# Kernel optimization log

Hardware: AMD Instinct MI355X
Metric: run time of the kernel (lower is better)

Reference implementation:

```python
import jax, jax.numpy as jnp
import numpy as np

B, L, HID = 2, 2048, 4096
NH, NKV, HD = 16, 4, 64
BLOCK = 16
THETA = 8000000.0
EPS = 1e-6
NEG = jnp.finfo(jnp.float32).min


def _rope_tables(theta, L, hd):
    inv_freq = 1.0 / (theta ** (np.arange(0, hd, 2, dtype=np.float32) / hd))  # [hd/2]
    t = np.arange(L, dtype=np.float32)
    freqs = np.outer(t, inv_freq)                      # [L, hd/2]
    emb = np.concatenate([freqs, freqs], axis=-1)      # [L, hd]
    return jnp.asarray(np.cos(emb)), jnp.asarray(np.sin(emb))


def setup_inputs() -> dict:
    key = jax.random.key(0)
    k1, k2, k3 = jax.random.split(key, 3)
    hidden_states = jax.random.normal(k1, (B, L, HID), dtype=jnp.float32)
    Wqkv = jax.random.normal(k2, (HID, (NH + 2 * NKV) * HD), dtype=jnp.float32) * 0.006
    Wo = jax.random.normal(k3, (NH * HD, HID), dtype=jnp.float32) * 0.006
    q_norm_w = jnp.ones((HD,), dtype=jnp.float32)
    k_norm_w = jnp.ones((HD,), dtype=jnp.float32)
    # block-diagonal causal additive mask [1,1,L,L]
    idx = jnp.arange(L)
    same_block = (idx[:, None] // BLOCK) == (idx[None, :] // BLOCK)
    causal = idx[:, None] >= idx[None, :]
    attention_mask = jnp.where(same_block & causal, 0.0, NEG)[None, None].astype(jnp.float32)
    cos1, sin1 = _rope_tables(THETA, L, HD)
    cos = jnp.broadcast_to(cos1[None], (B, L, HD))
    sin = jnp.broadcast_to(sin1[None], (B, L, HD))
    return {"hidden_states": hidden_states, "attention_mask": attention_mask,
            "cos": cos, "sin": sin, "Wqkv": Wqkv, "Wo": Wo,
            "q_norm_w": q_norm_w, "k_norm_w": k_norm_w}


def _rms_norm(x, w):
    xf = x.astype(jnp.float32)
    var = jnp.mean(xf * xf, axis=-1, keepdims=True)
    return (xf * jax.lax.rsqrt(var + EPS)).astype(x.dtype) * w


def _rotate_half(x):
    x1, x2 = jnp.split(x, 2, axis=-1)
    return jnp.concatenate([-x2, x1], axis=-1)


def reference(hidden_states, attention_mask, cos, sin, Wqkv, Wo, q_norm_w, k_norm_w):
    Bc, Lc, _ = hidden_states.shape
    qkv = hidden_states @ Wqkv                                # [B,L,(NH+2NKV)*HD]
    qkv = qkv.reshape(Bc, Lc, NH + 2 * NKV, HD)
    q, k, v = jnp.split(qkv, [NH, NH + NKV], axis=2)
    q = q.transpose(0, 2, 1, 3)                               # [B,NH,L,HD]
    k = k.transpose(0, 2, 1, 3)                               # [B,NKV,L,HD]
    v = v.transpose(0, 2, 1, 3)
    q = _rms_norm(q, q_norm_w)
    k = _rms_norm(k, k_norm_w)
    c = cos[:, None]                                          # [B,1,L,HD]
    s = sin[:, None]
    q = q * c + _rotate_half(q) * s
    k = k * c + _rotate_half(k) * s
    groups = NH // NKV
    k = jnp.repeat(k, groups, axis=1)                         # [B,NH,L,HD]
    v = jnp.repeat(v, groups, axis=1)
    scale = 1.0 / jnp.sqrt(jnp.float32(HD))
    scores = jnp.einsum('bhqd,bhkd->bhqk', q, k) * scale + attention_mask
    probs = jax.nn.softmax(scores, axis=-1)
    out = jnp.einsum('bhqk,bhkd->bhqd', probs, v)             # [B,NH,L,HD]
    out = out.transpose(0, 2, 1, 3).reshape(Bc, Lc, NH * HD)
    return out @ Wo
```

## Files before the change

kernel.cpp:

```cpp
#include <hip/hip_runtime.h>
#include <hip/hip_bf16.h>
#include <cstdint>

#define B_SZ   2
#define L_SEQ  2048
#define HID    4096
#define NH     16
#define NKV    4
#define HD     64
#define NQKV   (NH + 2*NKV)
#define QKV_N  (NQKV*HD)
#define O_N    (NH*HD)
#define M_ROWS (B_SZ*L_SEQ)
#define EPSV   1e-6f

typedef __bf16  bf16x8_t  __attribute__((ext_vector_type(8)));
typedef float   f32x4_t   __attribute__((ext_vector_type(4)));
typedef unsigned short ushort8_t __attribute__((ext_vector_type(8)));

__device__ __forceinline__ unsigned short f2b(float f) {
    union { float f; uint32_t u; } v; v.f = f;
    uint32_t r = v.u + 0x7FFFu + ((v.u >> 16) & 1u);
    return (unsigned short)(r >> 16);
}

__device__ __forceinline__ void gload_lds16(const void* g, void* l) {
    __builtin_amdgcn_global_load_lds(
        (__attribute__((address_space(1))) void*)(g),
        (__attribute__((address_space(3))) void*)(l),
        16, 0, 0);
}

#define BARF() do { asm volatile("" ::: "memory"); \
                    __builtin_amdgcn_s_barrier();  \
                    asm volatile("" ::: "memory"); } while (0)
#define LGKM0() do { asm volatile("s_waitcnt lgkmcnt(0)" ::: "memory"); \
                     __builtin_amdgcn_sched_barrier(0); } while (0)
#define VMC4()  asm volatile("s_waitcnt vmcnt(4)" ::: "memory")
#define VMC0()  asm volatile("s_waitcnt vmcnt(0)" ::: "memory")

__global__ __launch_bounds__(256) void cvt_f32_bf16(const float* __restrict__ in,
                                                    unsigned short* __restrict__ out,
                                                    int n8) {
    int i = blockIdx.x * 256 + threadIdx.x;
    if (i >= n8) return;
    const float4* p = (const float4*)(in + (size_t)i * 8);
    float4 a = p[0], b = p[1];
    ushort8_t o;
    o[0]=f2b(a.x); o[1]=f2b(a.y); o[2]=f2b(a.z); o[3]=f2b(a.w);
    o[4]=f2b(b.x); o[5]=f2b(b.y); o[6]=f2b(b.z); o[7]=f2b(b.w);
    *(ushort8_t*)(out + (size_t)i * 8) = o;
}

__global__ __launch_bounds__(256) void transpose_f32_bf16(const float* __restrict__ in,
                                                          unsigned short* __restrict__ out,
                                                          int R, int C) {
    __shared__ float t[32][33];
    const int c0 = blockIdx.x * 32;
    const int r0 = blockIdx.y * 32;
    const int tx = threadIdx.x & 31;
    const int ty = threadIdx.x >> 5;
    #pragma unroll
    for (int i = 0; i < 32; i += 8)
        t[ty + i][tx] = in[(size_t)(r0 + ty + i) * C + c0 + tx];
    __syncthreads();
    #pragma unroll
    for (int i = 0; i < 32; i += 8)
        out[(size_t)(c0 + ty + i) * R + r0 + tx] = f2b(t[tx][ty + i]);
}

__global__ __launch_bounds__(512, 2) void gemm256_bf16(const unsigned short* __restrict__ A,
                                                       const unsigned short* __restrict__ Bt,
                                                       float* __restrict__ C,
                                                       int M, int N, int K) {
    __shared__ unsigned short smem[65536];

    const int tid  = threadIdx.x;
    const int lane = tid & 63;
    const int wave = tid >> 6;
    const int wr   = wave >> 2;
    const int wc   = wave & 3;
    const int fr   = lane & 15;
    const int fq   = lane >> 4;

    const int nbx = N >> 8;
    int bid = blockIdx.x;
    const int cpx = gridDim.x >> 3;
    bid = (bid & 7) * cpx + (bid >> 3);
    const int bx = bid % nbx, by = bid / nbx;
    const int m0 = by << 8, n0 = bx << 8;

    const int srow = tid >> 3;
    const int scs  = ((tid & 7) ^ (srow & 7)) << 3;
    const unsigned short* gA = A  + (size_t)(m0 + srow) * K + scs;
    const unsigned short* gB = Bt + (size_t)(n0 + srow) * K + scs;

    const int cx0 = ((fq)     ^ (fr & 7)) << 3;
    const int cx1 = ((4 | fq) ^ (fr & 7)) << 3;

    f32x4_t acc[8][4];
    #pragma unroll
    for (int m = 0; m < 8; m++)
        #pragma unroll
        for (int n = 0; n < 4; n++)
            acc[m][n] = (f32x4_t){0.f, 0.f, 0.f, 0.f};

    bf16x8_t aF[2][2];
    bf16x8_t bF[4][2];

#define STG_A2(T, H) { _Pragma("unroll") for (int q = 0; q < 2; ++q) \
    gload_lds16(gA + (size_t)((H)*128 + q*64) * K + ((size_t)(T) << 6), \
                &smem[(((T)&1)<<15) + ((H)*128 + q*64)*64 + tid*8]); }
#define STG_B2(T, H) { _Pragma("unroll") for (int q = 0; q < 2; ++q) \
    gload_lds16(gB + (size_t)((H)*128 + q*64) * K + ((size_t)(T) << 6), \
                &smem[(((T)&1)<<15) + 16384 + ((H)*128 + q*64)*64 + tid*8]); }
#define RD_B2(SB) { _Pragma("unroll") for (int nn = 0; nn < 4; ++nn) { \
    const int ro = (SB) + 16384 + (wc*64 + nn*16 + fr)*64; \
    bF[nn][0] = *(const bf16x8_t*)&smem[ro + cx0]; \
    bF[nn][1] = *(const bf16x8_t*)&smem[ro + cx1]; } }
#define RD_A2(SB, P) { _Pragma("unroll") for (int m2 = 0; m2 < 2; ++m2) { \
    const int ro = (SB) + (wr*128 + ((P)*2 + m2)*16 + fr)*64; \
    aF[m2][0] = *(const bf16x8_t*)&smem[ro + cx0]; \
    aF[m2][1] = *(const bf16x8_t*)&smem[ro + cx1]; } }
#define MM2(P) { __builtin_amdgcn_s_setprio(1); \
    _Pragma("unroll") for (int m2 = 0; m2 < 2; ++m2) \
    _Pragma("unroll") for (int nn = 0; nn < 4; ++nn) \
    _Pragma("unroll") for (int kk = 0; kk < 2; ++kk) \
        acc[(P)*2 + m2][nn] = __builtin_amdgcn_mfma_f32_16x16x32_bf16( \
            aF[m2][kk], bF[nn][kk], acc[(P)*2 + m2][nn], 0, 0, 0); \
    __builtin_amdgcn_s_setprio(0); }

    const int NT = K >> 6;
    STG_A2(0, 0); STG_A2(0, 1); STG_B2(0, 0); STG_B2(0, 1);
    STG_B2(1, 0); STG_B2(1, 1);
    VMC4();
    BARF();

    for (int t = 0; t < NT; ++t) {
        const int sb = (t & 1) << 15;
        RD_B2(sb); RD_A2(sb, 0);
        if (t + 1 < NT) STG_A2(t + 1, 0);
        BARF(); LGKM0(); MM2(0); BARF();
        RD_A2(sb, 1);
        if (t + 1 < NT) STG_A2(t + 1, 1);
        BARF(); LGKM0(); MM2(1); BARF();
        RD_A2(sb, 2);
        if (t + 2 < NT) STG_B2(t + 2, 0);
        BARF(); LGKM0(); MM2(2); BARF();
        RD_A2(sb, 3);
        if (t + 2 < NT) STG_B2(t + 2, 1);
        BARF(); LGKM0(); MM2(3);
        if (t + 2 < NT) { VMC4(); } else { VMC0(); }
        BARF();
    }

    const int crow = m0 + wr * 128 + fq * 4;
    const int ccol = n0 + wc * 64 + fr;
    #pragma unroll
    for (int m = 0; m < 8; m++)
        #pragma unroll
        for (int n = 0; n < 4; n++)
            #pragma unroll
            for (int rr = 0; rr < 4; rr++)
                C[(size_t)(crow + m*16 + rr) * N + ccol + n*16] = acc[m][n][rr];
#undef STG_A2
#undef STG_B2
#undef RD_B2
#undef RD_A2
#undef MM2
}

__global__ __launch_bounds__(512, 2) void gemm256x128_bf16(const unsigned short* __restrict__ A,
                                                           const unsigned short* __restrict__ Bt,
                                                           float* __restrict__ C,
                                                           int M, int N, int K) {
    __shared__ unsigned short smem[49152];

    const int tid  = threadIdx.x;
    const int lane = tid & 63;
    const int wave = tid >> 6;
    const int wq   = wave >> 1;
    const int wn   = wave & 1;
    const int fr   = lane & 15;
    const int fq   = lane >> 4;

    const int nbx = N >> 7;
    int bid = blockIdx.x;
    const int cpx = gridDim.x >> 3;
    bid = (bid & 7) * cpx + (bid >> 3);
    const int bx = bid % nbx, by = bid / nbx;
    const int m0 = by << 8, n0 = bx << 7;

    const int srow = tid >> 3;
    const int scs  = ((tid & 7) ^ (srow & 7)) << 3;
    const unsigned short* gA = A  + (size_t)(m0 + srow) * K + scs;
    const unsigned short* gB = Bt + (size_t)(n0 + srow) * K + scs;

    const int cx0 = ((fq)     ^ (fr & 7)) << 3;
    const int cx1 = ((4 | fq) ^ (fr & 7)) << 3;

    f32x4_t acc[4][4];
    #pragma unroll
    for (int m = 0; m < 4; m++)
        #pragma unroll
        for (int n = 0; n < 4; n++)
            acc[m][n] = (f32x4_t){0.f, 0.f, 0.f, 0.f};

    bf16x8_t aF[4][2];
    bf16x8_t bF[4][2];

#define STG_A1(T, H) { _Pragma("unroll") for (int q = 0; q < 2; ++q) \
    gload_lds16(gA + (size_t)((H)*128 + q*64) * K + ((size_t)(T) << 6), \
                &smem[((T)&1)*24576 + ((H)*128 + q*64)*64 + tid*8]); }
#define STG_B1(T) { _Pragma("unroll") for (int q = 0; q < 2; ++q) \
    gload_lds16(gB + (size_t)(q*64) * K + ((size_t)(T) << 6), \
                &smem[((T)&1)*24576 + 16384 + q*4096 + tid*8]); }
#define RD_A1(SB, MM) { _Pragma("unroll") for (int m2 = 0; m2 < 2; ++m2) { \
    const int ro = (SB) + (wq*64 + ((MM) + m2)*16 + fr)*64; \
    aF[(MM)+m2][0] = *(const bf16x8_t*)&smem[ro + cx0]; \
    aF[(MM)+m2][1] = *(const bf16x8_t*)&smem[ro + cx1]; } }
#define RD_B1(SB, NN) { _Pragma("unroll") for (int n2 = 0; n2 < 2; ++n2) { \
    const int ro = (SB) + 16384 + (wn*64 + ((NN) + n2)*16 + fr)*64; \
    bF[(NN)+n2][0] = *(const bf16x8_t*)&smem[ro + cx0]; \
    bF[(NN)+n2][1] = *(const bf16x8_t*)&smem[ro + cx1]; } }
#define MM1(MH, NH) { __builtin_amdgcn_s_setprio(1); \
    _Pragma("unroll") for (int m2 = 0; m2 < 2; ++m2) \
    _Pragma("unroll") for (int n2 = 0; n2 < 2; ++n2) \
    _Pragma("unroll") for (int kk = 0; kk < 2; ++kk) \
        acc[(MH)*2 + m2][(NH)*2 + n2] = __builtin_amdgcn_mfma_f32_16x16x32_bf16( \
            aF[(MH)*2 + m2][kk], bF[(NH)*2 + n2][kk], acc[(MH)*2 + m2][(NH)*2 + n2], 0, 0, 0); \
    __builtin_amdgcn_s_setprio(0); }

    const int NT = K >> 6;
    STG_A1(0, 0); STG_A1(0, 1); STG_B1(0);
    STG_B1(1); STG_A1(1, 0);
    VMC4();
    BARF();

    for (int t = 0; t < NT; ++t) {
        const int sb = (t & 1) * 24576;
        RD_A1(sb, 0); RD_B1(sb, 0);
        if (t + 1 < NT) STG_A1(t + 1, 1);
        BARF(); LGKM0(); MM1(0, 0); BARF();
        RD_B1(sb, 2);
        BARF(); LGKM0(); MM1(0, 1); BARF();
        RD_A1(sb, 2);
        if (t + 2 < NT) STG_B1(t + 2);
        BARF(); LGKM0(); MM1(1, 1); BARF();
        if (t + 2 < NT) STG_A1(t + 2, 0);
        BARF(); LGKM0(); MM1(1, 0);
        if (t + 2 < NT) { VMC4(); } else { VMC0(); }
        BARF();
    }

    const int crow = m0 + wq * 64 + fq * 4;
    const int ccol = n0 + wn * 64 + fr;
    #pragma unroll
    for (int m = 0; m < 4; m++)
        #pragma unroll
        for (int n = 0; n < 4; n++)
            #pragma unroll
            for (int rr = 0; rr < 4; rr++)
                C[(size_t)(crow + m*16 + rr) * N + ccol + n*16] = acc[m][n][rr];
#undef STG_A1
#undef STG_B1
#undef RD_A1
#undef RD_B1
#undef MM1
}

__global__ __launch_bounds__(64) void attn_fused(const float* __restrict__ qkv,
                                                 const float* __restrict__ cosb,
                                                 const float* __restrict__ sinb,
                                                 const float* __restrict__ qw,
                                                 const float* __restrict__ kw,
                                                 unsigned short* __restrict__ out) {
    const int h    = blockIdx.x & (NH - 1);
    const int blk  = (blockIdx.x >> 4) & 127;
    const int b    = blockIdx.x >> 11;
    const int pos0 = blk * 16;
    const int kvh  = h >> 2;

    const int lane = threadIdx.x;
    const int r    = lane >> 2;
    const int qp   = lane & 3;
    const int d0   = qp * 16;

    __shared__ float qs[16][65];
    __shared__ float ks[16][65];
    __shared__ float vs[16][65];
    __shared__ float ps[16][17];

    const size_t rowb = ((size_t)(b * L_SEQ + pos0 + r)) * NQKV;
    const float* qptr = qkv + (rowb + h) * HD + d0;
    const float* kptr = qkv + (rowb + NH + kvh) * HD + d0;
    const float* vptr = qkv + (rowb + NH + NKV + kvh) * HD + d0;
    const size_t csrow = ((size_t)(b * L_SEQ + pos0 + r)) * HD + d0;

    float q[16], k[16], v[16], cs[16], sn[16];
    #pragma unroll
    for (int i = 0; i < 16; i += 4) {
        *(float4*)&q[i]  = *(const float4*)&qptr[i];
        *(float4*)&k[i]  = *(const float4*)&kptr[i];
        *(float4*)&v[i]  = *(const float4*)&vptr[i];
        *(float4*)&cs[i] = *(const float4*)&cosb[csrow + i];
        *(float4*)&sn[i] = *(const float4*)&sinb[csrow + i];
    }

    float sq = 0.f, sk = 0.f;
    #pragma unroll
    for (int i = 0; i < 16; i++) { sq += q[i]*q[i]; sk += k[i]*k[i]; }
    sq += __shfl_xor(sq, 1); sq += __shfl_xor(sq, 2);
    sk += __shfl_xor(sk, 1); sk += __shfl_xor(sk, 2);
    const float rq = rsqrtf(sq * (1.f / HD) + EPSV);
    const float rk = rsqrtf(sk * (1.f / HD) + EPSV);

    const float sgn = (qp < 2) ? -1.f : 1.f;
    #pragma unroll
    for (int i = 0; i < 16; i++) {
        float qn = q[i] * rq * qw[d0 + i];
        float kn = k[i] * rk * kw[d0 + i];
        float qo = __shfl_xor(qn, 2);
        float ko = __shfl_xor(kn, 2);
        qs[r][d0 + i] = qn * cs[i] + sgn * qo * sn[i];
        ks[r][d0 + i] = kn * cs[i] + sgn * ko * sn[i];
        vs[r][d0 + i] = v[i];
    }
    __syncthreads();

    float sc[4] = {0.f, 0.f, 0.f, 0.f};
    for (int d = 0; d < 64; d++) {
        const float qd = qs[r][d];
        sc[0] += qd * ks[qp     ][d];
        sc[1] += qd * ks[qp +  4][d];
        sc[2] += qd * ks[qp +  8][d];
        sc[3] += qd * ks[qp + 12][d];
    }
    #pragma unroll
    for (int cc = 0; cc < 4; cc++) {
        const int c = qp + cc * 4;
        sc[cc] = (c <= r) ? sc[cc] * 0.125f : -3.0e38f;
    }
    float mx = fmaxf(fmaxf(sc[0], sc[1]), fmaxf(sc[2], sc[3]));
    mx = fmaxf(mx, __shfl_xor(mx, 1));
    mx = fmaxf(mx, __shfl_xor(mx, 2));
    float e[4], sum = 0.f;
    #pragma unroll
    for (int cc = 0; cc < 4; cc++) { e[cc] = __expf(sc[cc] - mx); sum += e[cc]; }
    sum += __shfl_xor(sum, 1); sum += __shfl_xor(sum, 2);
    const float inv = 1.f / sum;
    #pragma unroll
    for (int cc = 0; cc < 4; cc++) ps[r][qp + cc * 4] = e[cc] * inv;
    __syncthreads();

    float o[16];
    #pragma unroll
    for (int i = 0; i < 16; i++) o[i] = 0.f;
    #pragma unroll
    for (int c = 0; c < 16; c++) {
        const float p = ps[r][c];
        #pragma unroll
        for (int i = 0; i < 16; i++) o[i] += p * vs[c][d0 + i];
    }

    __attribute__((aligned(16))) unsigned short ob[16];
    #pragma unroll
    for (int i = 0; i < 16; i++) ob[i] = f2b(o[i]);
    unsigned short* optr = out + (((size_t)(b * L_SEQ + pos0 + r) * NH + h) * HD) + d0;
    *(uint4*)optr       = *(uint4*)&ob[0];
    *((uint4*)optr + 1) = *(uint4*)&ob[8];
}

extern "C" void kernel_launch(void* const* d_in, const int* in_sizes, int n_in,
                              void* d_out, int out_size, void* d_ws, size_t ws_size,
                              hipStream_t stream) {
    const float* hid  = (const float*)d_in[0];
    const float* cosb = (const float*)d_in[2];
    const float* sinb = (const float*)d_in[3];
    const float* Wqkv = (const float*)d_in[4];
    const float* Wo   = (const float*)d_in[5];
    const float* qw   = (const float*)d_in[6];
    const float* kw   = (const float*)d_in[7];
    float* outp = (float*)d_out;

    char* ws = (char*)d_ws;
    unsigned short* Hb    = (unsigned short*)ws; ws += (size_t)M_ROWS * HID * 2;
    unsigned short* WqkvT = (unsigned short*)ws; ws += (size_t)QKV_N * HID * 2;
    unsigned short* WoT   = (unsigned short*)ws; ws += (size_t)HID * O_N * 2;
    float*          qkvf  = (float*)ws;          ws += (size_t)M_ROWS * QKV_N * 4;
    unsigned short* attnb = (unsigned short*)ws;

    {
        int n8 = (M_ROWS * HID) / 8;
        cvt_f32_bf16<<<(n8 + 255) / 256, 256, 0, stream>>>(hid, Hb, n8);
    }
    transpose_f32_bf16<<<dim3(QKV_N / 32, HID / 32), 256, 0, stream>>>(Wqkv, WqkvT, HID, QKV_N);
    transpose_f32_bf16<<<dim3(HID / 32, O_N / 32),  256, 0, stream>>>(Wo,   WoT,   O_N, HID);
    gemm256x128_bf16<<<dim3((M_ROWS / 256) * (QKV_N / 128)), 512, 0, stream>>>(Hb, WqkvT, qkvf, M_ROWS, QKV_N, HID);
    attn_fused<<<dim3(B_SZ * (L_SEQ / 16) * NH), 64, 0, stream>>>(qkvf, cosb, sinb, qw, kw, attnb);
    gemm256_bf16<<<dim3((M_ROWS / 256) * (HID / 256)), 512, 0, stream>>>(attnb, WoT, outp, M_ROWS, HID, O_N);
}
```

Before: 161.8 us.

## Triple-buffer QKV GEMM pipeline and store QKV intermediate in bf16

The QKV GEMM moves from a two-stage LDS buffer with staggered A/B staging to a three-stage ring. Each stage is loaded whole two iterations ahead, so each k-step needs only two MFMA phases with fewer barriers, and all A fragments are loaded at once. The QKV output is now written as bf16 instead of fp32, which halves the intermediate traffic, and the attention kernel reads and unpacks bf16. In exchange, LDS use grows to 144KB per block, which may limit occupancy with launch bounds of (512,2), and q/k/v lose precision before the norm.

```diff
diff --git a/kernel.cpp b/kernel.cpp
--- a/kernel.cpp
+++ b/kernel.cpp
@@ -23,6 +23,10 @@
     uint32_t r = v.u + 0x7FFFu + ((v.u >> 16) & 1u);
     return (unsigned short)(r >> 16);
 }
+__device__ __forceinline__ float b2f(unsigned short u) {
+    union { uint32_t u; float f; } v; v.u = ((uint32_t)u) << 16;
+    return v.f;
+}
 
 __device__ __forceinline__ void gload_lds16(const void* g, void* l) {
     __builtin_amdgcn_global_load_lds(
@@ -36,6 +40,7 @@
                     asm volatile("" ::: "memory"); } while (0)
 #define LGKM0() do { asm volatile("s_waitcnt lgkmcnt(0)" ::: "memory"); \
                      __builtin_amdgcn_sched_barrier(0); } while (0)
+#define VMC6()  asm volatile("s_waitcnt vmcnt(6)" ::: "memory")
 #define VMC4()  asm volatile("s_waitcnt vmcnt(4)" ::: "memory")
 #define VMC0()  asm volatile("s_waitcnt vmcnt(0)" ::: "memory")
 
@@ -172,9 +177,9 @@
 
 __global__ __launch_bounds__(512, 2) void gemm256x128_bf16(const unsigned short* __restrict__ A,
                                                            const unsigned short* __restrict__ Bt,
-                                                           float* __restrict__ C,
+                                                           unsigned short* __restrict__ C,
                                                            int M, int N, int K) {
-    __shared__ unsigned short smem[49152];
+    __shared__ unsigned short smem[73728];
 
     const int tid  = threadIdx.x;
     const int lane = tid & 63;
@@ -207,49 +212,45 @@
             acc[m][n] = (f32x4_t){0.f, 0.f, 0.f, 0.f};
 
     bf16x8_t aF[4][2];
-    bf16x8_t bF[4][2];
-
-#define STG_A1(T, H) { _Pragma("unroll") for (int q = 0; q < 2; ++q) \
-    gload_lds16(gA + (size_t)((H)*128 + q*64) * K + ((size_t)(T) << 6), \
-                &smem[((T)&1)*24576 + ((H)*128 + q*64)*64 + tid*8]); }
-#define STG_B1(T) { _Pragma("unroll") for (int q = 0; q < 2; ++q) \
-    gload_lds16(gB + (size_t)(q*64) * K + ((size_t)(T) << 6), \
-                &smem[((T)&1)*24576 + 16384 + q*4096 + tid*8]); }
-#define RD_A1(SB, MM) { _Pragma("unroll") for (int m2 = 0; m2 < 2; ++m2) { \
-    const int ro = (SB) + (wq*64 + ((MM) + m2)*16 + fr)*64; \
-    aF[(MM)+m2][0] = *(const bf16x8_t*)&smem[ro + cx0]; \
-    aF[(MM)+m2][1] = *(const bf16x8_t*)&smem[ro + cx1]; } }
+    bf16x8_t bF[2][2];
+
+#define STG_T1(T) { const int pb = ((T)%3)*24576; \
+    _Pragma("unroll") for (int q = 0; q < 4; ++q) \
+        gload_lds16(gA + (size_t)(q*64)*K + ((size_t)(T) << 6), \
+                    &smem[pb + q*4096 + tid*8]); \
+    _Pragma("unroll") for (int q = 0; q < 2; ++q) \
+        gload_lds16(gB + (size_t)(q*64)*K + ((size_t)(T) << 6), \
+                    &smem[pb + 16384 + q*4096 + tid*8]); }
+#define RD_A1(SB) { _Pragma("unroll") for (int mm = 0; mm < 4; ++mm) { \
+    const int ro = (SB) + (wq*64 + mm*16 + fr)*64; \
+    aF[mm][0] = *(const bf16x8_t*)&smem[ro + cx0]; \
+    aF[mm][1] = *(const bf16x8_t*)&smem[ro + cx1]; } }
 #define RD_B1(SB, NN) { _Pragma("unroll") for (int n2 = 0; n2 < 2; ++n2) { \
     const int ro = (SB) + 16384 + (wn*64 + ((NN) + n2)*16 + fr)*64; \
-    bF[(NN)+n2][0] = *(const bf16x8_t*)&smem[ro + cx0]; \
-    bF[(NN)+n2][1] = *(const bf16x8_t*)&smem[ro + cx1]; } }
-#define MM1(MH, NH) { __builtin_amdgcn_s_setprio(1); \
-    _Pragma("unroll") for (int m2 = 0; m2 < 2; ++m2) \
+    bF[n2][0] = *(const bf16x8_t*)&smem[ro + cx0]; \
+    bF[n2][1] = *(const bf16x8_t*)&smem[ro + cx1]; } }
+#define MM1(NH_) { __builtin_amdgcn_s_setprio(1); \
+    _Pragma("unroll") for (int mm = 0; mm < 4; ++mm) \
     _Pragma("unroll") for (int n2 = 0; n2 < 2; ++n2) \
     _Pragma("unroll") for (int kk = 0; kk < 2; ++kk) \
-        acc[(MH)*2 + m2][(NH)*2 + n2] = __builtin_amdgcn_mfma_f32_16x16x32_bf16( \
-            aF[(MH)*2 + m2][kk], bF[(NH)*2 + n2][kk], acc[(MH)*2 + m2][(NH)*2 + n2], 0, 0, 0); \
+        acc[mm][(NH_)*2 + n2] = __builtin_amdgcn_mfma_f32_16x16x32_bf16( \
+            aF[mm][kk], bF[n2][kk], acc[mm][(NH_)*2 + n2], 0, 0, 0); \
     __builtin_amdgcn_s_setprio(0); }
 
     const int NT = K >> 6;
-    STG_A1(0, 0); STG_A1(0, 1); STG_B1(0);
-    STG_B1(1); STG_A1(1, 0);
-    VMC4();
+    STG_T1(0);
+    STG_T1(1);
+    VMC6();
     BARF();
 
     for (int t = 0; t < NT; ++t) {
-        const int sb = (t & 1) * 24576;
-        RD_A1(sb, 0); RD_B1(sb, 0);
-        if (t + 1 < NT) STG_A1(t + 1, 1);
-        BARF(); LGKM0(); MM1(0, 0); BARF();
+        const int sb = (t % 3) * 24576;
+        RD_A1(sb); RD_B1(sb, 0);
+        if (t + 2 < NT) STG_T1(t + 2);
+        BARF(); LGKM0(); MM1(0); BARF();
         RD_B1(sb, 2);
-        BARF(); LGKM0(); MM1(0, 1); BARF();
-        RD_A1(sb, 2);
-        if (t + 2 < NT) STG_B1(t + 2);
-        BARF(); LGKM0(); MM1(1, 1); BARF();
-        if (t + 2 < NT) STG_A1(t + 2, 0);
-        BARF(); LGKM0(); MM1(1, 0);
-        if (t + 2 < NT) { VMC4(); } else { VMC0(); }
+        BARF(); LGKM0(); MM1(1);
+        if (t + 2 < NT) { VMC6(); } else if (t + 1 < NT) { VMC0(); }
         BARF();
     }
 
@@ -261,15 +262,14 @@
         for (int n = 0; n < 4; n++)
             #pragma unroll
             for (int rr = 0; rr < 4; rr++)
-                C[(size_t)(crow + m*16 + rr) * N + ccol + n*16] = acc[m][n][rr];
-#undef STG_A1
-#undef STG_B1
+                C[(size_t)(crow + m*16 + rr) * N + ccol + n*16] = f2b(acc[m][n][rr]);
+#undef STG_T1
 #undef RD_A1
 #undef RD_B1
 #undef MM1
 }
 
-__global__ __launch_bounds__(64) void attn_fused(const float* __restrict__ qkv,
+__global__ __launch_bounds__(64) void attn_fused(const unsigned short* __restrict__ qkv,
                                                  const float* __restrict__ cosb,
                                                  const float* __restrict__ sinb,
                                                  const float* __restrict__ qw,
@@ -292,19 +292,27 @@
     __shared__ float ps[16][17];
 
     const size_t rowb = ((size_t)(b * L_SEQ + pos0 + r)) * NQKV;
-    const float* qptr = qkv + (rowb + h) * HD + d0;
-    const float* kptr = qkv + (rowb + NH + kvh) * HD + d0;
-    const float* vptr = qkv + (rowb + NH + NKV + kvh) * HD + d0;
+    const unsigned short* qptr = qkv + (rowb + h) * HD + d0;
+    const unsigned short* kptr = qkv + (rowb + NH + kvh) * HD + d0;
+    const unsigned short* vptr = qkv + (rowb + NH + NKV + kvh) * HD + d0;
     const size_t csrow = ((size_t)(b * L_SEQ + pos0 + r)) * HD + d0;
 
     float q[16], k[16], v[16], cs[16], sn[16];
-    #pragma unroll
-    for (int i = 0; i < 16; i += 4) {
-        *(float4*)&q[i]  = *(const float4*)&qptr[i];
-        *(float4*)&k[i]  = *(const float4*)&kptr[i];
-        *(float4*)&v[i]  = *(const float4*)&vptr[i];
-        *(float4*)&cs[i] = *(const float4*)&cosb[csrow + i];
-        *(float4*)&sn[i] = *(const float4*)&sinb[csrow + i];
+    {
+        ushort8_t q0 = *(const ushort8_t*)&qptr[0], q1 = *(const ushort8_t*)&qptr[8];
+        ushort8_t k0 = *(const ushort8_t*)&kptr[0], k1 = *(const ushort8_t*)&kptr[8];
+        ushort8_t v0 = *(const ushort8_t*)&vptr[0], v1 = *(const ushort8_t*)&vptr[8];
+        #pragma unroll
+        for (int i = 0; i < 8; i++) {
+            q[i] = b2f(q0[i]); q[i+8] = b2f(q1[i]);
+            k[i] = b2f(k0[i]); k[i+8] = b2f(k1[i]);
+            v[i] = b2f(v0[i]); v[i+8] = b2f(v1[i]);
+        }
+        #pragma unroll
+        for (int i = 0; i < 16; i += 4) {
+            *(float4*)&cs[i] = *(const float4*)&cosb[csrow + i];
+            *(float4*)&sn[i] = *(const float4*)&sinb[csrow + i];
+        }
     }
 
     float sq = 0.f, sk = 0.f;
@@ -387,7 +395,7 @@
     unsigned short* Hb    = (unsigned short*)ws; ws += (size_t)M_ROWS * HID * 2;
     unsigned short* WqkvT = (unsigned short*)ws; ws += (size_t)QKV_N * HID * 2;
     unsigned short* WoT   = (unsigned short*)ws; ws += (size_t)HID * O_N * 2;
-    float*          qkvf  = (float*)ws;          ws += (size_t)M_ROWS * QKV_N * 4;
+    unsigned short* qkvb  = (unsigned short*)ws; ws += (size_t)M_ROWS * QKV_N * 2;
     unsigned short* attnb = (unsigned short*)ws;
 
     {
@@ -396,7 +404,7 @@
     }
     transpose_f32_bf16<<<dim3(QKV_N / 32, HID / 32), 256, 0, stream>>>(Wqkv, WqkvT, HID, QKV_N);
     transpose_f32_bf16<<<dim3(HID / 32, O_N / 32),  256, 0, stream>>>(Wo,   WoT,   O_N, HID);
-    gemm256x128_bf16<<<dim3((M_ROWS / 256) * (QKV_N / 128)), 512, 0, stream>>>(Hb, WqkvT, qkvf, M_ROWS, QKV_N, HID);
-    attn_fused<<<dim3(B_SZ * (L_SEQ / 16) * NH), 64, 0, stream>>>(qkvf, cosb, sinb, qw, kw, attnb);
+    gemm256x128_bf16<<<dim3((M_ROWS / 256) * (QKV_N / 128)), 512, 0, stream>>>(Hb, WqkvT, qkvb, M_ROWS, QKV_N, HID);
+    attn_fused<<<dim3(B_SZ * (L_SEQ / 16) * NH), 64, 0, stream>>>(qkvb, cosb, sinb, qw, kw, attnb);
     gemm256_bf16<<<dim3((M_ROWS / 256) * (HID / 256)), 512, 0, stream>>>(attnb, WoT, outp, M_ROWS, HID, O_N);
 }
```

Measured after the change: 160.6 us. Within noise of the previous version (-0.7%).
